# Optimization experiments

Measured on AMD Instinct MI355X. Metric: run time of the kernel, lower is better.

## Reference

```python
import jax, jax.numpy as jnp
import numpy as np

EMB = 768
HID = 3072
HID2 = 2 * HID
NE = 8
K = 2
B, N = 8, 2048


def setup_inputs() -> dict:
    key = jax.random.key(0)
    ks = jax.random.split(key, 9)
    s = lambda *d: 1.0 / np.sqrt(d[-2])  # ~ torch Linear init scale
    inp = {
        'x': jax.random.normal(ks[0], (B, N, EMB), dtype=jnp.float32),
        'Wg': jax.random.normal(ks[1], (EMB, NE), dtype=jnp.float32) * (1.0 / np.sqrt(EMB)),
        'bg': jnp.zeros((NE,), dtype=jnp.float32),
        'W1': jax.random.normal(ks[2], (NE, EMB, HID), dtype=jnp.float32) * (1.0 / np.sqrt(EMB)),
        'b1': jnp.zeros((NE, HID), dtype=jnp.float32),
        'W2': jax.random.normal(ks[3], (NE, HID, HID2), dtype=jnp.float32) * (1.0 / np.sqrt(HID)),
        'b2': jnp.zeros((NE, HID2), dtype=jnp.float32),
        'W3': jax.random.normal(ks[4], (NE, HID2, EMB), dtype=jnp.float32) * (1.0 / np.sqrt(HID2)),
        'b3': jnp.zeros((NE, EMB), dtype=jnp.float32),
    }
    return inp


def _gelu(x):
    return jax.nn.gelu(x, approximate=False)  # torch nn.GELU default (erf)


def reference(x, Wg, bg, W1, b1, W2, b2, W3, b3):
    # gating: top-k over expert scores, softmax over the k selected logits
    scores = x @ Wg + bg                     # [B,N,NE]
    topk_vals, topk_idx = jax.lax.top_k(scores, K)   # [B,N,K]
    gates = jax.nn.softmax(topk_vals, axis=-1)       # [B,N,K]
    # dense combine weights: c[b,n,e] = sum_i gates[...,i] * (idx[...,i]==e)
    onehot = jax.nn.one_hot(topk_idx, NE, dtype=x.dtype)  # [B,N,K,NE]
    comb = jnp.einsum('bnk,bnke->bne', gates, onehot)     # [B,N,NE]
    out = jnp.zeros_like(x)
    for e in range(NE):  # small fixed expert loop
        h = _gelu(x @ W1[e] + b1[e])       # [B,N,HID]
        h = _gelu(h @ W2[e] + b2[e])       # [B,N,HID2]
        y = h @ W3[e] + b3[e]              # [B,N,EMB]
        out = out + comb[..., e:e + 1] * y
    return out
```

## Files before the change

kernel.cpp:

```cpp
#include <hip/hip_runtime.h>
#include <hip/hip_bf16.h>

#define EMB 768
#define HID 3072
#define HID2 6144
#define NE 8
#define TOK 16384
#define SLOTS 32768
#define SLACK 256
#define MAXTILES 136

typedef __attribute__((ext_vector_type(8))) short bf16x8;
typedef __attribute__((ext_vector_type(4))) float f32x4;

__device__ __forceinline__ unsigned short bfbits(float f) {
  __hip_bfloat16 h = __float2bfloat16(f);
  return __builtin_bit_cast(unsigned short, h);
}


__global__ void k_init(int* counts, int* fill) {
  if (threadIdx.x < NE) { counts[threadIdx.x] = 0; fill[threadIdx.x] = 0; }
}

__global__ __launch_bounds__(256) void k_gating(
    const float* __restrict__ x, const float* __restrict__ Wg,
    const float* __restrict__ bg, int* __restrict__ eidx,
    float* __restrict__ gates)
{
  const int wave = threadIdx.x >> 6, lane = threadIdx.x & 63;
  const int t = blockIdx.x * 4 + wave;
  const float* xr = x + (size_t)t * EMB;
  float p[NE];
#pragma unroll
  for (int e = 0; e < NE; ++e) p[e] = 0.f;
  for (int k = lane; k < EMB; k += 64) {
    const float xv = xr[k];
    const float* wr = Wg + (size_t)k * NE;
#pragma unroll
    for (int e = 0; e < NE; ++e) p[e] += xv * wr[e];
  }
#pragma unroll
  for (int e = 0; e < NE; ++e) {
#pragma unroll
    for (int o = 32; o > 0; o >>= 1) p[e] += __shfl_xor(p[e], o);
    p[e] += bg[e];
  }
  float v0 = -1e30f, v1 = -1e30f; int i0 = 0, i1 = 0;
#pragma unroll
  for (int e = 0; e < NE; ++e) {
    const float v = p[e];
    if (v > v0)      { v1 = v0; i1 = i0; v0 = v; i0 = e; }
    else if (v > v1) { v1 = v;  i1 = e; }
  }
  const float ex = expf(v1 - v0);
  const float g0 = 1.f / (1.f + ex);
  const float g1 = 1.f - g0;
  if (lane == 0) {
    eidx[2*t] = i0; eidx[2*t+1] = i1;
    gates[2*t] = g0; gates[2*t+1] = g1;
  }
}

__global__ __launch_bounds__(256) void k_count(const int* __restrict__ eidx,
                                               int* __restrict__ counts)
{
  __shared__ int bins[NE];
  if (threadIdx.x < NE) bins[threadIdx.x] = 0;
  __syncthreads();
  const int base = blockIdx.x * 512 + threadIdx.x * 2;
  atomicAdd(&bins[eidx[base]], 1);
  atomicAdd(&bins[eidx[base + 1]], 1);
  __syncthreads();
  if (threadIdx.x < NE) atomicAdd(&counts[threadIdx.x], bins[threadIdx.x]);
}

__global__ void k_offsets(const int* __restrict__ counts, int* __restrict__ offsets,
                          int* __restrict__ tmap)
{
  offsets[0] = 0;
  int idx = 0;
  for (int e = 0; e < NE; ++e) {
    offsets[e+1] = offsets[e] + counts[e];
    const int nt = (counts[e] + 255) >> 8;
    for (int i = 0; i < nt; ++i) tmap[idx++] = (e << 16) | i;
  }
  for (; idx < MAXTILES; ++idx) tmap[idx] = -1;
}

__global__ __launch_bounds__(256) void k_route(
    const int* __restrict__ eidx, int* __restrict__ fill,
    const int* __restrict__ offsets, int* __restrict__ route_tok,
    float* __restrict__ gate_slot, int* __restrict__ tok_k,
    const float* __restrict__ gates)
{
  __shared__ int bins[NE], base[NE];
  const int tid = threadIdx.x;
  if (tid < NE) bins[tid] = 0;
  __syncthreads();
  const int t = blockIdx.x * 256 + tid;
  int e0 = eidx[2*t], e1 = eidx[2*t+1];
  int lp0 = atomicAdd(&bins[e0], 1);
  int lp1 = atomicAdd(&bins[e1], 1);
  __syncthreads();
  if (tid < NE) base[tid] = atomicAdd(&fill[tid], bins[tid]);
  __syncthreads();
  const int s0 = offsets[e0] + base[e0] + lp0;
  const int s1 = offsets[e1] + base[e1] + lp1;
  route_tok[s0] = t;          route_tok[s1] = t;
  gate_slot[s0] = gates[2*t]; gate_slot[s1] = gates[2*t+1];
  tok_k[s0] = 2*t;            tok_k[s1] = 2*t + 1;
}

__global__ __launch_bounds__(256) void k_gather(
    const float* __restrict__ x, const int* __restrict__ route_tok,
    __hip_bfloat16* __restrict__ xg)
{
  const int w = threadIdx.x >> 6, lane = threadIdx.x & 63;
  const int s = blockIdx.x * 4 + w;
  const int t = route_tok[s];
  const float4* src = (const float4*)(x + (size_t)t * EMB);
  unsigned short* dst = (unsigned short*)xg + (size_t)s * EMB;
#pragma unroll
  for (int i = 0; i < 3; ++i) {
    const float4 v = src[lane + 64 * i];
    ushort4 u;
    u.x = bfbits(v.x); u.y = bfbits(v.y); u.z = bfbits(v.z); u.w = bfbits(v.w);
    *(ushort4*)(dst + (lane + 64 * i) * 4) = u;
  }
}

#define NT1 (NE * (HID  / 64) * (EMB  / 64))
#define NT2 (NE * (HID2 / 64) * (HID  / 64))
#define NT3 (NE * (EMB  / 64) * (HID2 / 64))

typedef __attribute__((ext_vector_type(8))) unsigned short u16x8;

__global__ __launch_bounds__(256) void k_transpose_all(
    const float* __restrict__ W1, const float* __restrict__ W2,
    const float* __restrict__ W3, __hip_bfloat16* __restrict__ Wb1,
    __hip_bfloat16* __restrict__ Wb2, __hip_bfloat16* __restrict__ Wb3)
{
  __shared__ float tile[64][65];
  int bid = blockIdx.x;
  const float* W; __hip_bfloat16* Wt; int K, N;
  if (bid < NT1)              { W = W1; Wt = Wb1; K = EMB;  N = HID;  }
  else if (bid < NT1 + NT2)   { W = W2; Wt = Wb2; K = HID;  N = HID2; bid -= NT1; }
  else                        { W = W3; Wt = Wb3; K = HID2; N = EMB;  bid -= NT1 + NT2; }
  const int ntn = N >> 6, ntk = K >> 6;
  const int e  = bid / (ntn * ntk);
  const int rem = bid - e * (ntn * ntk);
  const int k0 = (rem / ntn) << 6;
  const int n0 = (rem % ntn) << 6;

  const float* Wp = W + (size_t)e * K * N;
  __hip_bfloat16* Wtp = Wt + (size_t)e * K * N;
  const int tx = threadIdx.x, ty = threadIdx.y;

  const int q = tx & 15, rsub = tx >> 4;
#pragma unroll
  for (int it = 0; it < 4; ++it) {
    const int r = it * 16 + ty * 2 + rsub;
    const float4 v = *(const float4*)(Wp + (size_t)(k0 + r) * N + n0 + 4 * q);
    tile[r][4 * q]     = v.x;
    tile[r][4 * q + 1] = v.y;
    tile[r][4 * q + 2] = v.z;
    tile[r][4 * q + 3] = v.w;
  }
  __syncthreads();
  const int q8 = tx & 7, r8 = tx >> 3;
#pragma unroll
  for (int it = 0; it < 2; ++it) {
    const int n = it * 32 + ty * 4 + r8;
    u16x8 u;
#pragma unroll
    for (int j = 0; j < 8; ++j) u[j] = bfbits(tile[8 * q8 + j][n]);
    *(u16x8*)((unsigned short*)Wtp + (size_t)(n0 + n) * K + k0 + 8 * q8) = u;
  }
}


#define BARRIER() asm volatile("s_barrier" ::: "memory")
#define LGKM(n) { asm volatile("s_waitcnt lgkmcnt(" #n ")" ::: "memory"); __builtin_amdgcn_sched_barrier(0); }
#define VMC(n)  { asm volatile("s_waitcnt vmcnt(" #n ")" ::: "memory"); __builtin_amdgcn_sched_barrier(0); }

template<bool GELU, bool OUTBF, bool ATOMIC>
__global__ __launch_bounds__(512) void ffn_gemm8(
    const __hip_bfloat16* __restrict__ A,
    const __hip_bfloat16* __restrict__ Bt,
    const float* __restrict__ bias,
    void* __restrict__ Cout,
    const int* __restrict__ counts,
    const int* __restrict__ offsets,
    const int* __restrict__ tmap,
    const float* __restrict__ gate_slot,
    const int* __restrict__ tok_k,
    int K, int N, int KLEN)
{
  const int me = tmap[blockIdx.y];
  if (me < 0) return;
  const int e  = me >> 16;
  const int m0 = (me & 0xffff) << 8;
  const int cnt = counts[e];
  const int seg = offsets[e];
  const int n0 = blockIdx.x * 256;
  const int kbase = blockIdx.z * KLEN * 2;

  __shared__ char lds[131072];

  const int tid = threadIdx.x;
  const int wave = tid >> 6, lane = tid & 63;
  const int wm = wave >> 2, wn = wave & 3;

  const size_t KB = (size_t)K * 2;
  const char* Ag = (const char*)(A + (size_t)(seg + m0) * K);
  const char* Bg = (const char*)(Bt + (size_t)e * N * K + (size_t)n0 * K);

  const int s_r  = tid >> 2;
  const int s_cb = ((tid & 3) * 16) ^ (((s_r >> 1) & 3) << 4);

  auto S = [&](int x) {
    const int ub = (x & 3) * 32768;
    const int kbyte = kbase + x * 64;
    const char* sa = Ag + (size_t)s_r * KB + kbyte + s_cb;
    const char* sb = Bg + (size_t)s_r * KB + kbyte + s_cb;
    __builtin_amdgcn_global_load_lds(
        (const __attribute__((address_space(1))) void*)sa,
        (__attribute__((address_space(3))) void*)(lds + ub + tid * 16), 16, 0, 0);
    __builtin_amdgcn_global_load_lds(
        (const __attribute__((address_space(1))) void*)(sa + 128 * KB),
        (__attribute__((address_space(3))) void*)(lds + ub + 8192 + tid * 16), 16, 0, 0);
    __builtin_amdgcn_global_load_lds(
        (const __attribute__((address_space(1))) void*)sb,
        (__attribute__((address_space(3))) void*)(lds + ub + 16384 + tid * 16), 16, 0, 0);
    __builtin_amdgcn_global_load_lds(
        (const __attribute__((address_space(1))) void*)(sb + 128 * KB),
        (__attribute__((address_space(3))) void*)(lds + ub + 16384 + 8192 + tid * 16), 16, 0, 0);
  };

  const int fr    = lane & 15;
  const int coff  = ((lane >> 4) * 16) ^ (((fr >> 1) & 3) << 4);
  const int aoff0 = (wm * 128 + fr) * 64 + coff;
  const int boff0 = 16384 + (wn * 64 + fr) * 64 + coff;

  f32x4 acc[8][4];
#pragma unroll
  for (int i = 0; i < 8; ++i)
#pragma unroll
    for (int j = 0; j < 4; ++j)
      acc[i][j] = (f32x4){0.f, 0.f, 0.f, 0.f};

  const int NPH = KLEN >> 5;

  bf16x8 aE[8], bE[4], aO[8], bO[4];

#define RD(x, as, bs) {                                             \
    const char* ub_ = lds + ((x) & 3) * 32768;                      \
    _Pragma("unroll")                                               \
    for (int m_ = 0; m_ < 8; ++m_)                                  \
      as[m_] = *(const bf16x8*)(ub_ + aoff0 + m_ * 1024);           \
    _Pragma("unroll")                                               \
    for (int n_ = 0; n_ < 4; ++n_)                                  \
      bs[n_] = *(const bf16x8*)(ub_ + boff0 + n_ * 1024); }

#define MM(as, bs) {                                                \
    _Pragma("unroll")                                               \
    for (int m_ = 0; m_ < 8; ++m_)                                  \
      _Pragma("unroll")                                             \
      for (int n_ = 0; n_ < 4; ++n_)                                \
        acc[m_][n_] = __builtin_amdgcn_mfma_f32_16x16x32_bf16(      \
            as[m_], bs[n_], acc[m_][n_], 0, 0, 0); }

  S(0); S(1);
  VMC(4);
  BARRIER();

  RD(0, aE, bE);
  S(2);
  VMC(4);
  BARRIER();

  RD(1, aO, bO);
  S(3);
  LGKM(12);
  MM(aE, bE);
  VMC(4);
  BARRIER();

  for (int p = 2; p < NPH; p += 2) {
    RD(p, aE, bE);
    S(p + 2 < NPH ? p + 2 : NPH - 1);
    LGKM(12);
    MM(aO, bO);
    VMC(4);
    BARRIER();
    RD(p + 1, aO, bO);
    S(p + 3 < NPH ? p + 3 : NPH - 1);
    LGKM(12);
    MM(aE, bE);
    VMC(4);
    BARRIER();
  }

  LGKM(0);
  MM(aO, bO);

#undef RD
#undef MM

#pragma unroll
  for (int mf = 0; mf < 8; ++mf) {
#pragma unroll
    for (int r2 = 0; r2 < 4; ++r2) {
      const int gm = m0 + wm * 128 + mf * 16 + (lane >> 4) * 4 + r2;
      if (gm >= cnt) continue;
      if (ATOMIC) {
        const int s = seg + gm;
        const float g = gate_slot[s];
        const int tok = tok_k[s] >> 1;
        float* dst = (float*)Cout + (size_t)tok * EMB;
        const bool addb = (blockIdx.z == 0);
#pragma unroll
        for (int nf = 0; nf < 4; ++nf) {
          const int gcol = n0 + wn * 64 + nf * 16 + fr;
          const float v = acc[mf][nf][r2] + (addb ? bias[(size_t)e * N + gcol] : 0.f);
          atomicAdd(&dst[gcol], g * v);
        }
      } else {
#pragma unroll
        for (int nf = 0; nf < 4; ++nf) {
          const int gcol = n0 + wn * 64 + nf * 16 + fr;
          float v = acc[mf][nf][r2] + bias[(size_t)e * N + gcol];
          if (GELU) v = 0.5f * v * (1.0f + erff(v * 0.70710678118654752f));
          if (OUTBF)
            ((__hip_bfloat16*)Cout)[(size_t)(seg + gm) * N + gcol] = __float2bfloat16(v);
          else
            ((float*)Cout)[(size_t)(seg + gm) * N + gcol] = v;
        }
      }
    }
  }
}


extern "C" void kernel_launch(void* const* d_in, const int* in_sizes, int n_in,
                              void* d_out, int out_size, void* d_ws, size_t ws_size,
                              hipStream_t stream)
{
  const float* x  = (const float*)d_in[0];
  const float* Wg = (const float*)d_in[1];
  const float* bg = (const float*)d_in[2];
  const float* W1 = (const float*)d_in[3];
  const float* b1 = (const float*)d_in[4];
  const float* W2 = (const float*)d_in[5];
  const float* b2 = (const float*)d_in[6];
  const float* W3 = (const float*)d_in[7];
  const float* b3 = (const float*)d_in[8];
  float* out = (float*)d_out;

  char* ws = (char*)d_ws;
  size_t off = 0;
  auto alloc = [&](size_t bytes) -> void* {
    void* p = ws + off;
    off = (off + bytes + 255) & ~(size_t)255;
    return p;
  };

  int*   counts    = (int*)alloc(NE * 4);
  int*   fill      = (int*)alloc(NE * 4);
  int*   offsets   = (int*)alloc((NE + 1) * 4);
  int*   tmap      = (int*)alloc(MAXTILES * 4);
  int*   eidx      = (int*)alloc((size_t)TOK * 2 * 4);
  float* gates     = (float*)alloc((size_t)TOK * 2 * 4);
  int*   route_tok = (int*)alloc((size_t)SLOTS * 4);
  float* gate_slot = (float*)alloc((size_t)(SLOTS + SLACK) * 4);
  int*   tok_k     = (int*)alloc((size_t)(SLOTS + SLACK) * 4);
  __hip_bfloat16* Wb1 = (__hip_bfloat16*)alloc((size_t)NE * EMB  * HID  * 2);
  __hip_bfloat16* Wb2 = (__hip_bfloat16*)alloc((size_t)NE * HID  * HID2 * 2);
  __hip_bfloat16* Wb3 = (__hip_bfloat16*)alloc((size_t)NE * HID2 * EMB  * 2);
  __hip_bfloat16* xg  = (__hip_bfloat16*)alloc((size_t)(SLOTS + SLACK) * EMB  * 2);
  __hip_bfloat16* h1  = (__hip_bfloat16*)alloc((size_t)(SLOTS + SLACK) * HID  * 2);
  __hip_bfloat16* h2  = (__hip_bfloat16*)alloc((size_t)(SLOTS + SLACK) * HID2 * 2);
  (void)ws_size; (void)in_sizes; (void)n_in;

  hipMemsetAsync(d_out, 0, (size_t)out_size * 4, stream);

  k_init<<<1, 64, 0, stream>>>(counts, fill);
  k_gating<<<TOK / 4, 256, 0, stream>>>(x, Wg, bg, eidx, gates);
  k_count<<<SLOTS / 512, 256, 0, stream>>>(eidx, counts);
  k_offsets<<<1, 1, 0, stream>>>(counts, offsets, tmap);
  k_route<<<TOK / 256, 256, 0, stream>>>(eidx, fill, offsets, route_tok,
                                         gate_slot, tok_k, gates);
  k_gather<<<SLOTS / 4, 256, 0, stream>>>(x, route_tok, xg);

  k_transpose_all<<<NT1 + NT2 + NT3, dim3(32, 8), 0, stream>>>(W1, W2, W3, Wb1, Wb2, Wb3);

  ffn_gemm8<true,  true,  false><<<dim3(HID  / 256, MAXTILES), 512, 0, stream>>>(
      xg, Wb1, b1, h1, counts, offsets, tmap, nullptr, nullptr, EMB,  HID,  EMB);
  ffn_gemm8<true,  true,  false><<<dim3(HID2 / 256, MAXTILES), 512, 0, stream>>>(
      h1, Wb2, b2, h2, counts, offsets, tmap, nullptr, nullptr, HID,  HID2, HID);
  ffn_gemm8<false, false, true ><<<dim3(EMB  / 256, MAXTILES, 4), 512, 0, stream>>>(
      h2, Wb3, b3, out, counts, offsets, tmap, gate_slot, tok_k, HID2, EMB, HID2 / 4);
}
```

Baseline: 2.746 ms.

## Replace atomic split-K scatter with per-split buffers and a combine kernel

The third expert GEMM used to atomically add gated results into a zeroed output, with split-K of 4. It now writes plain stores into four separate float slabs, one per (split, top-k slot) pair, using split-K of 2. A new elementwise kernel then sums the four slabs into the output, and the output memset is removed. Separately, the MFMA block is wrapped in s_setprio to raise wave priority during matrix math. The aim is to drop contended fp32 atomics, at the cost of an extra 200 MB workspace buffer and a full read pass over it, plus less K-parallelism in the last GEMM.

Result: faster. 2.518 ms (-8.3%).

```diff
diff --git a/kernel.cpp b/kernel.cpp
--- a/kernel.cpp
+++ b/kernel.cpp
@@ -184,7 +184,7 @@
 #define LGKM(n) { asm volatile("s_waitcnt lgkmcnt(" #n ")" ::: "memory"); __builtin_amdgcn_sched_barrier(0); }
 #define VMC(n)  { asm volatile("s_waitcnt vmcnt(" #n ")" ::: "memory"); __builtin_amdgcn_sched_barrier(0); }
 
-template<bool GELU, bool OUTBF, bool ATOMIC>
+template<bool GELU, bool OUTBF, bool SCATTER>
 __global__ __launch_bounds__(512) void ffn_gemm8(
     const __hip_bfloat16* __restrict__ A,
     const __hip_bfloat16* __restrict__ Bt,
@@ -264,12 +264,14 @@
       bs[n_] = *(const bf16x8*)(ub_ + boff0 + n_ * 1024); }
 
 #define MM(as, bs) {                                                \
+    __builtin_amdgcn_s_setprio(1);                                  \
     _Pragma("unroll")                                               \
     for (int m_ = 0; m_ < 8; ++m_)                                  \
       _Pragma("unroll")                                             \
       for (int n_ = 0; n_ < 4; ++n_)                                \
         acc[m_][n_] = __builtin_amdgcn_mfma_f32_16x16x32_bf16(      \
-            as[m_], bs[n_], acc[m_][n_], 0, 0, 0); }
+            as[m_], bs[n_], acc[m_][n_], 0, 0, 0);                  \
+    __builtin_amdgcn_s_setprio(0); }
 
   S(0); S(1);
   VMC(4);
@@ -314,17 +316,17 @@
     for (int r2 = 0; r2 < 4; ++r2) {
       const int gm = m0 + wm * 128 + mf * 16 + (lane >> 4) * 4 + r2;
       if (gm >= cnt) continue;
-      if (ATOMIC) {
+      if (SCATTER) {
         const int s = seg + gm;
         const float g = gate_slot[s];
-        const int tok = tok_k[s] >> 1;
-        float* dst = (float*)Cout + (size_t)tok * EMB;
+        const int tk = tok_k[s];
+        float* dst = (float*)Cout +
+            ((size_t)(blockIdx.z * 2 + (tk & 1)) * TOK + (size_t)(tk >> 1)) * EMB;
         const bool addb = (blockIdx.z == 0);
 #pragma unroll
         for (int nf = 0; nf < 4; ++nf) {
           const int gcol = n0 + wn * 64 + nf * 16 + fr;
-          const float v = acc[mf][nf][r2] + (addb ? bias[(size_t)e * N + gcol] : 0.f);
-          atomicAdd(&dst[gcol], g * v);
+          dst[gcol] = g * (acc[mf][nf][r2] + (addb ? bias[(size_t)e * N + gcol] : 0.f));
         }
       } else {
 #pragma unroll
@@ -339,6 +341,25 @@
         }
       }
     }
+  }
+}
+
+__global__ __launch_bounds__(256) void k_combine4(const float* __restrict__ ybuf4,
+                                                  float* __restrict__ out)
+{
+  const size_t stride = (size_t)TOK * EMB;
+  const size_t total = stride / 4;
+  for (size_t i = blockIdx.x * 256 + threadIdx.x; i < total; i += (size_t)gridDim.x * 256) {
+    const float4 a = ((const float4*)ybuf4)[i];
+    const float4 b = ((const float4*)(ybuf4 + stride))[i];
+    const float4 c = ((const float4*)(ybuf4 + 2 * stride))[i];
+    const float4 d = ((const float4*)(ybuf4 + 3 * stride))[i];
+    float4 o;
+    o.x = (a.x + b.x) + (c.x + d.x);
+    o.y = (a.y + b.y) + (c.y + d.y);
+    o.z = (a.z + b.z) + (c.z + d.z);
+    o.w = (a.w + b.w) + (c.w + d.w);
+    ((float4*)out)[i] = o;
   }
 }
 
@@ -381,9 +402,8 @@
   __hip_bfloat16* xg  = (__hip_bfloat16*)alloc((size_t)(SLOTS + SLACK) * EMB  * 2);
   __hip_bfloat16* h1  = (__hip_bfloat16*)alloc((size_t)(SLOTS + SLACK) * HID  * 2);
   __hip_bfloat16* h2  = (__hip_bfloat16*)alloc((size_t)(SLOTS + SLACK) * HID2 * 2);
-  (void)ws_size; (void)in_sizes; (void)n_in;
-
-  hipMemsetAsync(d_out, 0, (size_t)out_size * 4, stream);
+  float*          ybuf4 = (float*)alloc((size_t)4 * TOK * EMB * 4);
+  (void)ws_size; (void)in_sizes; (void)n_in; (void)out_size;
 
   k_init<<<1, 64, 0, stream>>>(counts, fill);
   k_gating<<<TOK / 4, 256, 0, stream>>>(x, Wg, bg, eidx, gates);
@@ -399,6 +419,8 @@
       xg, Wb1, b1, h1, counts, offsets, tmap, nullptr, nullptr, EMB,  HID,  EMB);
   ffn_gemm8<true,  true,  false><<<dim3(HID2 / 256, MAXTILES), 512, 0, stream>>>(
       h1, Wb2, b2, h2, counts, offsets, tmap, nullptr, nullptr, HID,  HID2, HID);
-  ffn_gemm8<false, false, true ><<<dim3(EMB  / 256, MAXTILES, 4), 512, 0, stream>>>(
-      h2, Wb3, b3, out, counts, offsets, tmap, gate_slot, tok_k, HID2, EMB, HID2 / 4);
-}
+  ffn_gemm8<false, false, true ><<<dim3(EMB  / 256, MAXTILES, 2), 512, 0, stream>>>(
+      h2, Wb3, b3, ybuf4, counts, offsets, tmap, gate_slot, tok_k, HID2, EMB, HID2 / 2);
+
+  k_combine4<<<2048, 256, 0, stream>>>(ybuf4, out);
+}
```
